# Kernel optimization log

Hardware: AMD Instinct MI355X
Metric: run time of the kernel (lower is better)

## Reference

```python
import jax, jax.numpy as jnp
import numpy as np

N = 50000       # nodes
E = 800000      # edges
D_IN = 128      # input_dim
HID = 256       # hidden_dim
HEADS = 4
FH = HID // 4   # per-head out dim = 64
OUT = 8         # output_dim
NEG_SLOPE = 0.2 # GATConv leaky_relu slope


def setup_inputs() -> dict:
    key = jax.random.key(0)
    ks = jax.random.split(key, 16)
    def glorot(k, shape):
        fan_in, fan_out = shape[0], shape[-1]
        s = jnp.sqrt(6.0 / (fan_in + fan_out))
        return jax.random.uniform(k, shape, jnp.float32, -s, s)
    inp = {
        "x": jax.random.normal(ks[0], (N, D_IN), jnp.float32),
        "edge_index": jax.random.randint(ks[1], (2, E), 0, N, jnp.int64),
        # GCN layers
        "W1": glorot(ks[2], (D_IN, HID)), "b1": jnp.zeros((HID,), jnp.float32),
        "W2": glorot(ks[3], (HID, HID)), "b2": jnp.zeros((HID,), jnp.float32),
        "W3": glorot(ks[4], (HID, HID // 2)), "b3": jnp.zeros((HID // 2,), jnp.float32),
        # GAT layer: in = HID//2 = 128, out per head = FH, 4 heads concat -> HID
        "Wg": glorot(ks[5], (HID // 2, HEADS * FH)),
        "a_src": glorot(ks[6], (HEADS, FH)),
        "a_dst": glorot(ks[7], (HEADS, FH)),
        "bg": jnp.zeros((HEADS * FH,), jnp.float32),
        # classifier MLP: HID -> HID//2 -> HID//4 -> OUT
        "Wc1": glorot(ks[8], (HID, HID // 2)), "bc1": jnp.zeros((HID // 2,), jnp.float32),
        "Wc2": glorot(ks[9], (HID // 2, HID // 4)), "bc2": jnp.zeros((HID // 4,), jnp.float32),
        "Wc3": glorot(ks[10], (HID // 4, OUT)), "bc3": jnp.zeros((OUT,), jnp.float32),
    }
    return inp


def _with_self_loops(edge_index, n):
    loop = jnp.arange(n, dtype=edge_index.dtype)
    src = jnp.concatenate([edge_index[0], loop])
    dst = jnp.concatenate([edge_index[1], loop])
    return src, dst


def gcn_conv(x, W, b, src, dst, n):
    # PyG GCNConv: h = X W; out = D^{-1/2}(A+I)D^{-1/2} h + b (self loops in src/dst)
    h = x @ W
    deg = jax.ops.segment_sum(jnp.ones_like(dst, jnp.float32), dst, num_segments=n)
    dinv = jnp.where(deg > 0, jax.lax.rsqrt(deg), 0.0)
    norm = dinv[src] * dinv[dst]                      # [E+N]
    out = jax.ops.segment_sum(h[src] * norm[:, None], dst, num_segments=n)
    return out + b


def gat_conv(x, Wg, a_src, a_dst, bg, src, dst, n):
    # PyG GATConv (eval mode, no attn dropout), self loops included in src/dst
    h = (x @ Wg).reshape(n, HEADS, FH)                # [N,H,F]
    al_s = jnp.einsum('nhf,hf->nh', h, a_src)         # [N,H]
    al_d = jnp.einsum('nhf,hf->nh', h, a_dst)
    e = jax.nn.leaky_relu(al_s[src] + al_d[dst], NEG_SLOPE)  # [E+N,H]
    m = jax.ops.segment_max(e, dst, num_segments=n)   # per-dst stable softmax
    ex = jnp.exp(e - m[dst])
    den = jax.ops.segment_sum(ex, dst, num_segments=n)
    alpha = ex / den[dst]                             # [E+N,H]
    out = jax.ops.segment_sum(h[src] * alpha[:, :, None], dst, num_segments=n)
    return out.reshape(n, HEADS * FH) + bg


def reference(x, edge_index, W1, b1, W2, b2, W3, b3, Wg, a_src, a_dst, bg,
              Wc1, bc1, Wc2, bc2, Wc3, bc3):
    n = x.shape[0]
    src, dst = _with_self_loops(edge_index, n)
    h1 = jax.nn.relu(gcn_conv(x, W1, b1, src, dst, n))
    h2 = jax.nn.relu(gcn_conv(h1, W2, b2, src, dst, n)) + h1
    h3 = jax.nn.relu(gcn_conv(h2, W3, b3, src, dst, n))
    h_att = jax.nn.relu(gat_conv(h3, Wg, a_src, a_dst, bg, src, dst, n))
    h_pooled = jnp.mean(h_att, axis=0, keepdims=True)           # [1, HID]
    z = jax.nn.relu(h_pooled @ Wc1 + bc1)
    z = jax.nn.relu(z @ Wc2 + bc2)
    return z @ Wc3 + bc3                                        # [1, OUT]
```

## Files before the change

kernel.cpp:

```cpp
#include <hip/hip_runtime.h>
#include <hip/hip_bf16.h>

#define NNODES 50000
#define NEDGES 800000
#define EN 850000
#define SCAN_B 196

typedef __attribute__((ext_vector_type(8))) short bf16x8;
typedef __attribute__((ext_vector_type(4))) float f32x4;

__device__ __forceinline__ float bf2f(unsigned short u) {
    return __uint_as_float(((unsigned)u) << 16);
}
__device__ __forceinline__ float bflo(unsigned u) { return __uint_as_float(u << 16); }
__device__ __forceinline__ float bfhi(unsigned u) { return __uint_as_float(u & 0xffff0000u); }
__device__ __forceinline__ unsigned short f2bf(float x) {
    unsigned u = __float_as_uint(x);
    u += 0x7fffu + ((u >> 16) & 1u);
    return (unsigned short)(u >> 16);
}
__device__ __forceinline__ unsigned pack2bf(float a, float b) {
    return (unsigned)f2bf(a) | ((unsigned)f2bf(b) << 16);
}
__device__ __forceinline__ void acc8(float* acc, uint4 v, float wg) {
    acc[0] += bflo(v.x) * wg; acc[1] += bfhi(v.x) * wg;
    acc[2] += bflo(v.y) * wg; acc[3] += bfhi(v.y) * wg;
    acc[4] += bflo(v.z) * wg; acc[5] += bfhi(v.z) * wg;
    acc[6] += bflo(v.w) * wg; acc[7] += bfhi(v.w) * wg;
}

__device__ __forceinline__ void split_bf(float x, unsigned short& h, unsigned short& l) {
    unsigned u = __float_as_uint(x);
    h = (unsigned short)(u >> 16);
    float r = x - __uint_as_float(u & 0xffff0000u);
    l = (unsigned short)(__float_as_uint(r) >> 16);
}
__device__ __forceinline__ void do_split(const float* W, unsigned short* Wh, unsigned short* Wl,
                                         int i, int K, int N) {
    int n = i / K, k = i - n * K;
    unsigned short h, l;
    split_bf(W[(size_t)k * N + n], h, l);
    Wh[i] = h; Wl[i] = l;
}

__global__ __launch_bounds__(256) void prep_kernel(const int* __restrict__ ei, float* __restrict__ deg,
                                                   const float* __restrict__ x, unsigned short* __restrict__ xbf,
                                                   const float* __restrict__ W1, const float* __restrict__ W2,
                                                   const float* __restrict__ W3, const float* __restrict__ Wg,
                                                   unsigned short* __restrict__ W1th, unsigned short* __restrict__ W1tl,
                                                   unsigned short* __restrict__ W2th, unsigned short* __restrict__ W2tl,
                                                   unsigned short* __restrict__ W3th, unsigned short* __restrict__ W3tl,
                                                   unsigned short* __restrict__ Wgth, unsigned short* __restrict__ Wgtl) {
    int idx = blockIdx.x * 256 + threadIdx.x;
    atomicAdd(&deg[ei[NEDGES + idx]], 1.0f);
    {
        float4 a = *(const float4*)&x[(size_t)idx * 8];
        float4 b = *(const float4*)&x[(size_t)idx * 8 + 4];
        uint4 o;
        o.x = pack2bf(a.x, a.y); o.y = pack2bf(a.z, a.w);
        o.z = pack2bf(b.x, b.y); o.w = pack2bf(b.z, b.w);
        *(uint4*)&xbf[(size_t)idx * 8] = o;
    }
    if (idx < 32768)        do_split(W1, W1th, W1tl, idx, 128, 256);
    else if (idx < 98304)   do_split(W2, W2th, W2tl, idx - 32768, 256, 256);
    else if (idx < 131072)  do_split(W3, W3th, W3tl, idx - 98304, 256, 128);
    else if (idx < 163840)  do_split(Wg, Wgth, Wgtl, idx - 131072, 128, 256);
}

__global__ __launch_bounds__(256) void scan_part1(const float* __restrict__ deg, int* __restrict__ row,
                                                  int* __restrict__ bsum, float* __restrict__ dinv) {
    __shared__ int sdata[256];
    int t = threadIdx.x;
    int idx = blockIdx.x * 256 + t;
    float dg = idx < NNODES ? deg[idx] : 0.f;
    if (idx < NNODES) dinv[idx] = rsqrtf(dg + 1.0f);
    int v = idx < NNODES ? (int)dg + 1 : 0;
    sdata[t] = v;
    __syncthreads();
    for (int off = 1; off < 256; off <<= 1) {
        int tmp = t >= off ? sdata[t - off] : 0;
        __syncthreads();
        sdata[t] += tmp;
        __syncthreads();
    }
    if (idx < NNODES) row[idx] = sdata[t] - v;
    if (t == 255) bsum[blockIdx.x] = sdata[255];
}

__global__ __launch_bounds__(256) void scan_part2(int* __restrict__ bsum, int* __restrict__ bofs,
                                                  int* __restrict__ row) {
    __shared__ int sdata[256];
    int t = threadIdx.x;
    int v = t < SCAN_B ? bsum[t] : 0;
    sdata[t] = v;
    __syncthreads();
    for (int off = 1; off < 256; off <<= 1) {
        int tmp = t >= off ? sdata[t - off] : 0;
        __syncthreads();
        sdata[t] += tmp;
        __syncthreads();
    }
    if (t < SCAN_B) bofs[t] = sdata[t] - v;
    if (t == 0) row[NNODES] = EN;
}

__global__ __launch_bounds__(256) void scan_part3(int* __restrict__ row, const int* __restrict__ bofs) {
    int idx = blockIdx.x * 256 + threadIdx.x;
    if (idx < NNODES) row[idx] += bofs[blockIdx.x];
}

__global__ __launch_bounds__(256) void scatter_kernel(const int* __restrict__ ei, const int* __restrict__ row,
                                                      int* __restrict__ cursor, const float* __restrict__ dinv,
                                                      uint2* __restrict__ csr) {
    int e = blockIdx.x * blockDim.x + threadIdx.x;
    if (e >= EN) return;
    int s, d;
    if (e < NEDGES) { s = ei[e]; d = ei[NEDGES + e]; } else { s = e - NEDGES; d = s; }
    int pos = row[d] + atomicAdd(&cursor[d], 1);
    csr[pos] = make_uint2((unsigned)s, __float_as_uint(dinv[s] * dinv[d]));
}

template<int MODE>
__global__ __launch_bounds__(256) void gemm_bf(const unsigned short* __restrict__ A,
                                               const unsigned short* __restrict__ Wth,
                                               const unsigned short* __restrict__ Wtl,
                                               const float* __restrict__ bias,
                                               const float* __restrict__ asr, const float* __restrict__ ads,
                                               float* __restrict__ als, float* __restrict__ ald,
                                               unsigned short* __restrict__ C, int M, int K, int Nc) {
    __shared__ unsigned short As[128][40];
    __shared__ unsigned short Bh[128][40], Bl[128][40];
    int t = threadIdx.x;
    int row0 = blockIdx.x * 128, col0 = blockIdx.y * 128;
    int lane = t & 63, w = t >> 6;
    int mb = (w >> 1) * 64, nb = (w & 1) * 64;
    int lr = lane & 15, kg = (lane >> 4) * 8;

    f32x4 acc[4][4];
#pragma unroll
    for (int i = 0; i < 4; ++i)
#pragma unroll
        for (int j = 0; j < 4; ++j) acc[i][j] = (f32x4){0.f, 0.f, 0.f, 0.f};

    for (int k0 = 0; k0 < K; k0 += 32) {
#pragma unroll
        for (int it = 0; it < 2; ++it) {
            int q = it * 256 + t;
            int row = q >> 2, seg = (q & 3) * 8;
            int grow = row0 + row;
            uint4 v = make_uint4(0, 0, 0, 0);
            if (grow < M) v = *(const uint4*)&A[(size_t)grow * K + k0 + seg];
            *(uint4*)&As[row][seg] = v;
        }
#pragma unroll
        for (int it = 0; it < 2; ++it) {
            int o = it * 256 + t;
            int n = o >> 2, ko = (o & 3) * 8;
            size_t g = (size_t)(col0 + n) * K + k0 + ko;
            *(uint4*)&Bh[n][ko] = *(const uint4*)&Wth[g];
            *(uint4*)&Bl[n][ko] = *(const uint4*)&Wtl[g];
        }
        __syncthreads();

        bf16x8 a[4], bh[4], bl[4];
#pragma unroll
        for (int mf = 0; mf < 4; ++mf) a[mf] = *(const bf16x8*)&As[mb + mf * 16 + lr][kg];
#pragma unroll
        for (int nf = 0; nf < 4; ++nf) {
            bh[nf] = *(const bf16x8*)&Bh[nb + nf * 16 + lr][kg];
            bl[nf] = *(const bf16x8*)&Bl[nb + nf * 16 + lr][kg];
        }
#pragma unroll
        for (int mf = 0; mf < 4; ++mf)
#pragma unroll
            for (int nf = 0; nf < 4; ++nf) {
                acc[mf][nf] = __builtin_amdgcn_mfma_f32_16x16x32_bf16(a[mf], bh[nf], acc[mf][nf], 0, 0, 0);
                acc[mf][nf] = __builtin_amdgcn_mfma_f32_16x16x32_bf16(a[mf], bl[nf], acc[mf][nf], 0, 0, 0);
            }
        __syncthreads();
    }

    float s1[16], s2[16];
    if (MODE == 2) {
#pragma unroll
        for (int q = 0; q < 16; ++q) { s1[q] = 0.f; s2[q] = 0.f; }
    }

#pragma unroll
    for (int nf = 0; nf < 4; ++nf) {
        int col = col0 + nb + nf * 16 + lr;
        float bv = (MODE == 1) ? bias[col] : 0.f;
        float av = 0.f, dv = 0.f;
        if (MODE == 2) { av = asr[col]; dv = ads[col]; }
#pragma unroll
        for (int mf = 0; mf < 4; ++mf) {
#pragma unroll
            for (int r = 0; r < 4; ++r) {
                int row = row0 + mb + mf * 16 + (lane >> 4) * 4 + r;
                if (row < M) {
                    float v = acc[mf][nf][r];
                    if (MODE == 1) v = fmaxf(v + bv, 0.f);
                    C[(size_t)row * Nc + col] = f2bf(v);
                    if (MODE == 2) {
                        s1[mf * 4 + r] += v * av;
                        s2[mf * 4 + r] += v * dv;
                    }
                }
            }
        }
    }
    if (MODE == 2) {
        int head = (col0 + nb) >> 6;
#pragma unroll
        for (int q = 0; q < 16; ++q) {
#pragma unroll
            for (int off = 1; off < 16; off <<= 1) {
                s1[q] += __shfl_xor(s1[q], off);
                s2[q] += __shfl_xor(s2[q], off);
            }
        }
        if (lr == 0) {
#pragma unroll
            for (int mf = 0; mf < 4; ++mf) {
#pragma unroll
                for (int r = 0; r < 4; ++r) {
                    int row = row0 + mb + mf * 16 + (lane >> 4) * 4 + r;
                    if (row < M) {
                        als[row * 4 + head] = s1[mf * 4 + r];
                        ald[row * 4 + head] = s2[mf * 4 + r];
                    }
                }
            }
        }
    }
}

template<int NC, int MODE>
__global__ __launch_bounds__(256) void gcn_agg_bf(const unsigned short* __restrict__ h, const int* __restrict__ row,
                                                  const uint2* __restrict__ csr,
                                                  const float* __restrict__ b, const unsigned short* __restrict__ res,
                                                  unsigned short* __restrict__ out) {
    int wid = (int)((blockIdx.x * blockDim.x + threadIdx.x) >> 6);
    if (wid >= NNODES) return;
    int lane = threadIdx.x & 63;
    constexpr int LPE = NC / 8;
    constexpr int EPI = 64 / LPE;
    int sub = lane / LPE, li = lane % LPE;
    int col = li * 8;
    float acc[8];
#pragma unroll
    for (int i = 0; i < 8; ++i) acc[i] = 0.f;
    int j0 = row[wid], j1 = row[wid + 1];
    int j = j0 + sub;
    for (; j + 3 * EPI < j1; j += 4 * EPI) {
        uint2 c0 = csr[j], c1 = csr[j + EPI], c2 = csr[j + 2 * EPI], c3 = csr[j + 3 * EPI];
        uint4 v0 = *(const uint4*)&h[(size_t)c0.x * NC + col];
        uint4 v1 = *(const uint4*)&h[(size_t)c1.x * NC + col];
        uint4 v2 = *(const uint4*)&h[(size_t)c2.x * NC + col];
        uint4 v3 = *(const uint4*)&h[(size_t)c3.x * NC + col];
        acc8(acc, v0, __uint_as_float(c0.y));
        acc8(acc, v1, __uint_as_float(c1.y));
        acc8(acc, v2, __uint_as_float(c2.y));
        acc8(acc, v3, __uint_as_float(c3.y));
    }
    for (; j < j1; j += EPI) {
        uint2 c0 = csr[j];
        uint4 v0 = *(const uint4*)&h[(size_t)c0.x * NC + col];
        acc8(acc, v0, __uint_as_float(c0.y));
    }
#pragma unroll
    for (int i = 0; i < 8; ++i) {
        acc[i] += __shfl_xor(acc[i], 32);
        if constexpr (EPI == 4) acc[i] += __shfl_xor(acc[i], 16);
    }
    if (lane < LPE) {
        if constexpr (MODE >= 1) {
#pragma unroll
            for (int i = 0; i < 8; ++i) acc[i] = fmaxf(acc[i] + b[col + i], 0.f);
        }
        if constexpr (MODE == 2) {
            uint4 rv = *(const uint4*)&res[(size_t)wid * NC + col];
            acc8(acc, rv, 1.0f);
        }
        uint4 o;
        o.x = pack2bf(acc[0], acc[1]); o.y = pack2bf(acc[2], acc[3]);
        o.z = pack2bf(acc[4], acc[5]); o.w = pack2bf(acc[6], acc[7]);
        *(uint4*)&out[(size_t)wid * NC + col] = o;
    }
}

__device__ __forceinline__ float lrelu(float x) { return x < 0.f ? 0.2f * x : x; }

__global__ __launch_bounds__(256) void gat_csr(const unsigned short* __restrict__ hg, const int* __restrict__ row,
                                               const uint2* __restrict__ csr, const float* __restrict__ als,
                                               const float* __restrict__ ald, const float* __restrict__ bg,
                                               unsigned short* __restrict__ out) {
    __shared__ float alds[4][64][4];
    int wid = (int)((blockIdx.x * blockDim.x + threadIdx.x) >> 6);
    if (wid >= NNODES) return;
    int wv = threadIdx.x >> 6;
    int lane = threadIdx.x & 63;
    int j0 = row[wid], j1 = row[wid + 1];
    int deg = j1 - j0;
    float4 ad = *(const float4*)&ald[wid * 4];
    int sub = lane >> 5, li = lane & 31;
    int h = li >> 3;
    int col = li * 8;
    float acc[8];
#pragma unroll
    for (int i = 0; i < 8; ++i) acc[i] = 0.f;

    if (deg <= 64) {
        int sreg = 0;
        float e0 = -1e30f, e1 = -1e30f, e2 = -1e30f, e3 = -1e30f;
        if (lane < deg) {
            sreg = (int)csr[j0 + lane].x;
            float4 as4 = *(const float4*)&als[sreg * 4];
            e0 = lrelu(as4.x + ad.x); e1 = lrelu(as4.y + ad.y);
            e2 = lrelu(as4.z + ad.z); e3 = lrelu(as4.w + ad.w);
        }
        float m0 = e0, m1 = e1, m2 = e2, m3 = e3;
#pragma unroll
        for (int off = 32; off >= 1; off >>= 1) {
            m0 = fmaxf(m0, __shfl_xor(m0, off));
            m1 = fmaxf(m1, __shfl_xor(m1, off));
            m2 = fmaxf(m2, __shfl_xor(m2, off));
            m3 = fmaxf(m3, __shfl_xor(m3, off));
        }
        float x0 = __expf(e0 - m0), x1 = __expf(e1 - m1);
        float x2 = __expf(e2 - m2), x3 = __expf(e3 - m3);
        float d0 = x0, d1 = x1, d2 = x2, d3 = x3;
#pragma unroll
        for (int off = 32; off >= 1; off >>= 1) {
            d0 += __shfl_xor(d0, off);
            d1 += __shfl_xor(d1, off);
            d2 += __shfl_xor(d2, off);
            d3 += __shfl_xor(d3, off);
        }
        float i0 = 1.f / d0, i1 = 1.f / d1, i2 = 1.f / d2, i3 = 1.f / d3;
        *(float4*)&alds[wv][lane][0] = make_float4(x0 * i0, x1 * i1, x2 * i2, x3 * i3);
        int k = sub;
        for (; k + 6 < deg; k += 8) {
            int s0 = __shfl(sreg, k),     s1 = __shfl(sreg, k + 2);
            int s2 = __shfl(sreg, k + 4), s3 = __shfl(sreg, k + 6);
            float a0 = alds[wv][k][h],     a1 = alds[wv][k + 2][h];
            float a2 = alds[wv][k + 4][h], a3 = alds[wv][k + 6][h];
            uint4 v0 = *(const uint4*)&hg[(size_t)s0 * 256 + col];
            uint4 v1 = *(const uint4*)&hg[(size_t)s1 * 256 + col];
            uint4 v2 = *(const uint4*)&hg[(size_t)s2 * 256 + col];
            uint4 v3 = *(const uint4*)&hg[(size_t)s3 * 256 + col];
            acc8(acc, v0, a0); acc8(acc, v1, a1);
            acc8(acc, v2, a2); acc8(acc, v3, a3);
        }
        for (; k < deg; k += 2) {
            int s0 = __shfl(sreg, k);
            float a0 = alds[wv][k][h];
            uint4 v0 = *(const uint4*)&hg[(size_t)s0 * 256 + col];
            acc8(acc, v0, a0);
        }
    } else {
        float m0 = -1e30f, m1 = -1e30f, m2 = -1e30f, m3 = -1e30f;
        float d0 = 0.f, d1 = 0.f, d2 = 0.f, d3 = 0.f;
        for (int j = j0 + lane; j < j1; j += 64) {
            int s = (int)csr[j].x;
            float4 as4 = *(const float4*)&als[s * 4];
            m0 = fmaxf(m0, lrelu(as4.x + ad.x));
            m1 = fmaxf(m1, lrelu(as4.y + ad.y));
            m2 = fmaxf(m2, lrelu(as4.z + ad.z));
            m3 = fmaxf(m3, lrelu(as4.w + ad.w));
        }
#pragma unroll
        for (int off = 32; off >= 1; off >>= 1) {
            m0 = fmaxf(m0, __shfl_xor(m0, off));
            m1 = fmaxf(m1, __shfl_xor(m1, off));
            m2 = fmaxf(m2, __shfl_xor(m2, off));
            m3 = fmaxf(m3, __shfl_xor(m3, off));
        }
        for (int j = j0 + lane; j < j1; j += 64) {
            int s = (int)csr[j].x;
            float4 as4 = *(const float4*)&als[s * 4];
            d0 += __expf(lrelu(as4.x + ad.x) - m0);
            d1 += __expf(lrelu(as4.y + ad.y) - m1);
            d2 += __expf(lrelu(as4.z + ad.z) - m2);
            d3 += __expf(lrelu(as4.w + ad.w) - m3);
        }
#pragma unroll
        for (int off = 32; off >= 1; off >>= 1) {
            d0 += __shfl_xor(d0, off);
            d1 += __shfl_xor(d1, off);
            d2 += __shfl_xor(d2, off);
            d3 += __shfl_xor(d3, off);
        }
        float mh   = h == 0 ? m0 : h == 1 ? m1 : h == 2 ? m2 : m3;
        float invh = 1.f / (h == 0 ? d0 : h == 1 ? d1 : h == 2 ? d2 : d3);
        float adh  = h == 0 ? ad.x : h == 1 ? ad.y : h == 2 ? ad.z : ad.w;
        for (int j = j0 + sub; j < j1; j += 2) {
            uint2 c0 = csr[j];
            float a0 = __expf(lrelu(als[c0.x * 4 + h] + adh) - mh) * invh;
            uint4 v0 = *(const uint4*)&hg[(size_t)c0.x * 256 + col];
            acc8(acc, v0, a0);
        }
    }

#pragma unroll
    for (int i = 0; i < 8; ++i) acc[i] += __shfl_xor(acc[i], 32);
    if (lane < 32) {
        uint4 o;
        o.x = pack2bf(fmaxf(acc[0] + bg[col], 0.f),     fmaxf(acc[1] + bg[col + 1], 0.f));
        o.y = pack2bf(fmaxf(acc[2] + bg[col + 2], 0.f), fmaxf(acc[3] + bg[col + 3], 0.f));
        o.z = pack2bf(fmaxf(acc[4] + bg[col + 4], 0.f), fmaxf(acc[5] + bg[col + 5], 0.f));
        o.w = pack2bf(fmaxf(acc[6] + bg[col + 6], 0.f), fmaxf(acc[7] + bg[col + 7], 0.f));
        *(uint4*)&out[(size_t)wid * 256 + col] = o;
    }
}

__global__ __launch_bounds__(256) void pool_kernel(const unsigned short* __restrict__ hatt, float* __restrict__ ppart) {
    int col = threadIdx.x;
    int r0 = blockIdx.x * 256;
    int r1 = r0 + 256 < NNODES ? r0 + 256 : NNODES;
    float s = 0.f;
    for (int r = r0; r < r1; ++r) s += bf2f(hatt[(size_t)r * 256 + col]);
    ppart[blockIdx.x * 256 + col] = s;
}

__global__ __launch_bounds__(256) void mlp_kernel(const float* __restrict__ ppart,
                                                  const float* __restrict__ Wc1, const float* __restrict__ bc1,
                                                  const float* __restrict__ Wc2, const float* __restrict__ bc2,
                                                  const float* __restrict__ Wc3, const float* __restrict__ bc3,
                                                  float* __restrict__ out) {
    __shared__ float p[256], z1[128], z2[64];
    int t = threadIdx.x;
    float s0 = 0.f;
    for (int b = 0; b < SCAN_B; ++b) s0 += ppart[b * 256 + t];
    p[t] = s0 * (1.0f / NNODES);
    __syncthreads();
    if (t < 128) {
        float s = bc1[t];
        for (int k = 0; k < 256; ++k) s += p[k] * Wc1[k * 128 + t];
        z1[t] = fmaxf(s, 0.f);
    }
    __syncthreads();
    if (t < 64) {
        float s = bc2[t];
        for (int k = 0; k < 128; ++k) s += z1[k] * Wc2[k * 64 + t];
        z2[t] = fmaxf(s, 0.f);
    }
    __syncthreads();
    if (t < 8) {
        float s = bc3[t];
        for (int k = 0; k < 64; ++k) s += z2[k] * Wc3[k * 8 + t];
        out[t] = s;
    }
}

extern "C" void kernel_launch(void* const* d_in, const int* in_sizes, int n_in,
                              void* d_out, int out_size, void* d_ws, size_t ws_size,
                              hipStream_t stream) {
    const float* x   = (const float*)d_in[0];
    const int*   ei  = (const int*)d_in[1];
    const float* W1  = (const float*)d_in[2];  const float* b1  = (const float*)d_in[3];
    const float* W2  = (const float*)d_in[4];  const float* b2  = (const float*)d_in[5];
    const float* W3  = (const float*)d_in[6];  const float* b3  = (const float*)d_in[7];
    const float* Wg  = (const float*)d_in[8];
    const float* asr = (const float*)d_in[9];  const float* ads = (const float*)d_in[10];
    const float* bg  = (const float*)d_in[11];
    const float* Wc1 = (const float*)d_in[12]; const float* bc1 = (const float*)d_in[13];
    const float* Wc2 = (const float*)d_in[14]; const float* bc2 = (const float*)d_in[15];
    const float* Wc3 = (const float*)d_in[16]; const float* bc3 = (const float*)d_in[17];
    float* out = (float*)d_out;

    char* w = (char*)d_ws;
    float* deg    = (float*)w; w += (size_t)NNODES * 4;
    int*   cursor = (int*)w;   w += (size_t)NNODES * 4;
    float* dinv   = (float*)w; w += (size_t)NNODES * 4;
    int*   rowp   = (int*)w;   w += 200016;
    int*   bsum   = (int*)w;   w += 256 * 4;
    int*   bofs   = (int*)w;   w += 256 * 4;
    uint2* csr    = (uint2*)w; w += (size_t)EN * 8;
    float* als    = (float*)w; w += (size_t)NNODES * 4 * 4;
    float* ald    = (float*)w; w += (size_t)NNODES * 4 * 4;
    float* ppart  = (float*)w; w += (size_t)SCAN_B * 256 * 4;
    unsigned short* W1th = (unsigned short*)w; w += 128 * 256 * 2;
    unsigned short* W1tl = (unsigned short*)w; w += 128 * 256 * 2;
    unsigned short* W2th = (unsigned short*)w; w += 256 * 256 * 2;
    unsigned short* W2tl = (unsigned short*)w; w += 256 * 256 * 2;
    unsigned short* W3th = (unsigned short*)w; w += 256 * 128 * 2;
    unsigned short* W3tl = (unsigned short*)w; w += 256 * 128 * 2;
    unsigned short* Wgth = (unsigned short*)w; w += 128 * 256 * 2;
    unsigned short* Wgtl = (unsigned short*)w; w += 128 * 256 * 2;
    unsigned short* U1 = (unsigned short*)w; w += (size_t)NNODES * 256 * 2;
    unsigned short* U2 = (unsigned short*)w; w += (size_t)NNODES * 256 * 2;
    unsigned short* U3 = (unsigned short*)w; w += (size_t)NNODES * 256 * 2;
    unsigned short* U4 = (unsigned short*)w; w += (size_t)NNODES * 256 * 2;

    hipMemsetAsync(deg, 0, (size_t)NNODES * 8, stream);
    prep_kernel<<<3125, 256, 0, stream>>>(ei, deg, x, U1, W1, W2, W3, Wg,
                                          W1th, W1tl, W2th, W2tl, W3th, W3tl, Wgth, Wgtl);
    scan_part1<<<SCAN_B, 256, 0, stream>>>(deg, rowp, bsum, dinv);
    scan_part2<<<1, 256, 0, stream>>>(bsum, bofs, rowp);
    scan_part3<<<SCAN_B, 256, 0, stream>>>(rowp, bofs);
    scatter_kernel<<<(EN + 255) / 256, 256, 0, stream>>>(ei, rowp, cursor, dinv, csr);

    dim3 gA((NNODES + 127) / 128, 2);
    dim3 gB((NNODES + 127) / 128, 1);
    int aggBlocks = (NNODES * 64 + 255) / 256;

    gcn_agg_bf<128, 0><<<aggBlocks, 256, 0, stream>>>(U1, rowp, csr, nullptr, nullptr, U2);
    gemm_bf<1><<<gA, 256, 0, stream>>>(U2, W1th, W1tl, b1, nullptr, nullptr, nullptr, nullptr, U3, NNODES, 128, 256);

    gemm_bf<0><<<gA, 256, 0, stream>>>(U3, W2th, W2tl, nullptr, nullptr, nullptr, nullptr, nullptr, U1, NNODES, 256, 256);
    gcn_agg_bf<256, 2><<<aggBlocks, 256, 0, stream>>>(U1, rowp, csr, b2, U3, U2);

    gemm_bf<0><<<gB, 256, 0, stream>>>(U2, W3th, W3tl, nullptr, nullptr, nullptr, nullptr, nullptr, U4, NNODES, 256, 128);
    gcn_agg_bf<128, 1><<<aggBlocks, 256, 0, stream>>>(U4, rowp, csr, b3, nullptr, U1);

    gemm_bf<2><<<gA, 256, 0, stream>>>(U1, Wgth, Wgtl, nullptr, asr, ads, als, ald, U2, NNODES, 128, 256);
    gat_csr<<<aggBlocks, 256, 0, stream>>>(U2, rowp, csr, als, ald, bg, U3);

    pool_kernel<<<SCAN_B, 256, 0, stream>>>(U3, ppart);
    mlp_kernel<<<1, 256, 0, stream>>>(ppart, Wc1, bc1, Wc2, bc2, Wc3, bc3, out);
}
```

Measured before the change: 533.2 us.

## Reorder GAT layer to aggregate before projection, fold attention vectors into weights

The GAT layer is reassociated. Attention logits are computed directly from h3 using precomputed Wg·a_src and Wg·a_dst vectors, fused into the third GCN aggregation. Per-head weighted aggregation then runs over the 128-wide h3 rather than the 256-wide projected features, and a per-head GEMM with bias and relu follows. This removes the gather of 256-wide rows in GAT and the logit epilogue in the GEMM. In exchange it writes a 4x128-wide intermediate P and does more FMAs per edge. The scan_part3 launch is also dropped by adding block offsets at use sites.

```diff
diff --git a/kernel.cpp b/kernel.cpp
--- a/kernel.cpp
+++ b/kernel.cpp
@@ -28,6 +28,15 @@
     acc[4] += bflo(v.z) * wg; acc[5] += bfhi(v.z) * wg;
     acc[6] += bflo(v.w) * wg; acc[7] += bfhi(v.w) * wg;
 }
+__device__ __forceinline__ void accP(float (&a4)[4][8], uint4 v, float4 al) {
+    float f[8] = {bflo(v.x), bfhi(v.x), bflo(v.y), bfhi(v.y),
+                  bflo(v.z), bfhi(v.z), bflo(v.w), bfhi(v.w)};
+#pragma unroll
+    for (int i = 0; i < 8; ++i) {
+        a4[0][i] += f[i] * al.x; a4[1][i] += f[i] * al.y;
+        a4[2][i] += f[i] * al.z; a4[3][i] += f[i] * al.w;
+    }
+}
 
 __device__ __forceinline__ void split_bf(float x, unsigned short& h, unsigned short& l) {
     unsigned u = __float_as_uint(x);
@@ -47,10 +56,12 @@
                                                    const float* __restrict__ x, unsigned short* __restrict__ xbf,
                                                    const float* __restrict__ W1, const float* __restrict__ W2,
                                                    const float* __restrict__ W3, const float* __restrict__ Wg,
+                                                   const float* __restrict__ asr, const float* __restrict__ ads,
                                                    unsigned short* __restrict__ W1th, unsigned short* __restrict__ W1tl,
                                                    unsigned short* __restrict__ W2th, unsigned short* __restrict__ W2tl,
                                                    unsigned short* __restrict__ W3th, unsigned short* __restrict__ W3tl,
-                                                   unsigned short* __restrict__ Wgth, unsigned short* __restrict__ Wgtl) {
+                                                   unsigned short* __restrict__ Wgth, unsigned short* __restrict__ Wgtl,
+                                                   float* __restrict__ asp, float* __restrict__ adp) {
     int idx = blockIdx.x * 256 + threadIdx.x;
     atomicAdd(&deg[ei[NEDGES + idx]], 1.0f);
     {
@@ -65,6 +76,18 @@
     else if (idx < 98304)   do_split(W2, W2th, W2tl, idx - 32768, 256, 256);
     else if (idx < 131072)  do_split(W3, W3th, W3tl, idx - 98304, 256, 128);
     else if (idx < 163840)  do_split(Wg, Wgth, Wgtl, idx - 131072, 128, 256);
+    else if (idx < 164864) {
+        int i0 = idx - 163840;
+        int which = i0 >> 9;
+        int h = (i0 >> 7) & 3;
+        int k = i0 & 127;
+        const float* av = (which ? ads : asr) + h * 64;
+        const float* wg = Wg + (size_t)k * 256 + h * 64;
+        float s = 0.f;
+#pragma unroll
+        for (int c = 0; c < 64; ++c) s += wg[c] * av[c];
+        (which ? adp : asp)[h * 128 + k] = s;
+    }
 }
 
 __global__ __launch_bounds__(256) void scan_part1(const float* __restrict__ deg, int* __restrict__ row,
@@ -101,22 +124,18 @@
         __syncthreads();
     }
     if (t < SCAN_B) bofs[t] = sdata[t] - v;
-    if (t == 0) row[NNODES] = EN;
-}
-
-__global__ __launch_bounds__(256) void scan_part3(int* __restrict__ row, const int* __restrict__ bofs) {
-    int idx = blockIdx.x * 256 + threadIdx.x;
-    if (idx < NNODES) row[idx] += bofs[blockIdx.x];
+    if (t == SCAN_B - 1) row[NNODES] = EN - (sdata[t] - v);
 }
 
 __global__ __launch_bounds__(256) void scatter_kernel(const int* __restrict__ ei, const int* __restrict__ row,
+                                                      const int* __restrict__ bofs,
                                                       int* __restrict__ cursor, const float* __restrict__ dinv,
                                                       uint2* __restrict__ csr) {
     int e = blockIdx.x * blockDim.x + threadIdx.x;
     if (e >= EN) return;
     int s, d;
     if (e < NEDGES) { s = ei[e]; d = ei[NEDGES + e]; } else { s = e - NEDGES; d = s; }
-    int pos = row[d] + atomicAdd(&cursor[d], 1);
+    int pos = row[d] + bofs[d >> 8] + atomicAdd(&cursor[d], 1);
     csr[pos] = make_uint2((unsigned)s, __float_as_uint(dinv[s] * dinv[d]));
 }
 
@@ -125,8 +144,6 @@
                                                const unsigned short* __restrict__ Wth,
                                                const unsigned short* __restrict__ Wtl,
                                                const float* __restrict__ bias,
-                                               const float* __restrict__ asr, const float* __restrict__ ads,
-                                               float* __restrict__ als, float* __restrict__ ald,
                                                unsigned short* __restrict__ C, int M, int K, int Nc) {
     __shared__ unsigned short As[128][40];
     __shared__ unsigned short Bh[128][40], Bl[128][40];
@@ -180,18 +197,10 @@
         __syncthreads();
     }
 
-    float s1[16], s2[16];
-    if (MODE == 2) {
-#pragma unroll
-        for (int q = 0; q < 16; ++q) { s1[q] = 0.f; s2[q] = 0.f; }
-    }
-
 #pragma unroll
     for (int nf = 0; nf < 4; ++nf) {
         int col = col0 + nb + nf * 16 + lr;
         float bv = (MODE == 1) ? bias[col] : 0.f;
-        float av = 0.f, dv = 0.f;
-        if (MODE == 2) { av = asr[col]; dv = ads[col]; }
 #pragma unroll
         for (int mf = 0; mf < 4; ++mf) {
 #pragma unroll
@@ -201,35 +210,82 @@
                     float v = acc[mf][nf][r];
                     if (MODE == 1) v = fmaxf(v + bv, 0.f);
                     C[(size_t)row * Nc + col] = f2bf(v);
-                    if (MODE == 2) {
-                        s1[mf * 4 + r] += v * av;
-                        s2[mf * 4 + r] += v * dv;
-                    }
                 }
             }
         }
     }
-    if (MODE == 2) {
-        int head = (col0 + nb) >> 6;
-#pragma unroll
-        for (int q = 0; q < 16; ++q) {
-#pragma unroll
-            for (int off = 1; off < 16; off <<= 1) {
-                s1[q] += __shfl_xor(s1[q], off);
-                s2[q] += __shfl_xor(s2[q], off);
+}
+
+__global__ __launch_bounds__(256) void gemm_head(const unsigned short* __restrict__ P,
+                                                 const unsigned short* __restrict__ Wgth,
+                                                 const unsigned short* __restrict__ Wgtl,
+                                                 const float* __restrict__ bg,
+                                                 unsigned short* __restrict__ C) {
+    __shared__ unsigned short As[128][40];
+    __shared__ unsigned short Bh[64][40], Bl[64][40];
+    int t = threadIdx.x;
+    int head = blockIdx.y;
+    int row0 = blockIdx.x * 128;
+    const unsigned short* A  = P + (size_t)head * NNODES * 128;
+    const unsigned short* Wh = Wgth + head * 64 * 128;
+    const unsigned short* Wl = Wgtl + head * 64 * 128;
+    int lane = t & 63, w = t >> 6;
+    int mb = w * 32;
+    int lr = lane & 15, kg = (lane >> 4) * 8;
+
+    f32x4 acc[2][4];
+#pragma unroll
+    for (int i = 0; i < 2; ++i)
+#pragma unroll
+        for (int j = 0; j < 4; ++j) acc[i][j] = (f32x4){0.f, 0.f, 0.f, 0.f};
+
+    for (int k0 = 0; k0 < 128; k0 += 32) {
+#pragma unroll
+        for (int it = 0; it < 2; ++it) {
+            int q = it * 256 + t;
+            int row = q >> 2, seg = (q & 3) * 8;
+            int grow = row0 + row;
+            uint4 v = make_uint4(0, 0, 0, 0);
+            if (grow < NNODES) v = *(const uint4*)&A[(size_t)grow * 128 + k0 + seg];
+            *(uint4*)&As[row][seg] = v;
+        }
+        {
+            int n = t >> 2, ko = (t & 3) * 8;
+            size_t g = (size_t)n * 128 + k0 + ko;
+            *(uint4*)&Bh[n][ko] = *(const uint4*)&Wh[g];
+            *(uint4*)&Bl[n][ko] = *(const uint4*)&Wl[g];
+        }
+        __syncthreads();
+
+        bf16x8 a[2], bh[4], bl[4];
+#pragma unroll
+        for (int mf = 0; mf < 2; ++mf) a[mf] = *(const bf16x8*)&As[mb + mf * 16 + lr][kg];
+#pragma unroll
+        for (int nf = 0; nf < 4; ++nf) {
+            bh[nf] = *(const bf16x8*)&Bh[nf * 16 + lr][kg];
+            bl[nf] = *(const bf16x8*)&Bl[nf * 16 + lr][kg];
+        }
+#pragma unroll
+        for (int mf = 0; mf < 2; ++mf)
+#pragma unroll
+            for (int nf = 0; nf < 4; ++nf) {
+                acc[mf][nf] = __builtin_amdgcn_mfma_f32_16x16x32_bf16(a[mf], bh[nf], acc[mf][nf], 0, 0, 0);
+                acc[mf][nf] = __builtin_amdgcn_mfma_f32_16x16x32_bf16(a[mf], bl[nf], acc[mf][nf], 0, 0, 0);
             }
-        }
-        if (lr == 0) {
-#pragma unroll
-            for (int mf = 0; mf < 4; ++mf) {
-#pragma unroll
-                for (int r = 0; r < 4; ++r) {
-                    int row = row0 + mb + mf * 16 + (lane >> 4) * 4 + r;
-                    if (row < M) {
-                        als[row * 4 + head] = s1[mf * 4 + r];
-                        ald[row * 4 + head] = s2[mf * 4 + r];
-                    }
-                }
+        __syncthreads();
+    }
+
+#pragma unroll
+    for (int nf = 0; nf < 4; ++nf) {
+        int gcol = head * 64 + nf * 16 + lr;
+        float bv = bg[gcol];
+#pragma unroll
+        for (int mf = 0; mf < 2; ++mf) {
+#pragma unroll
+            for (int r = 0; r < 4; ++r) {
+                int row = row0 + mb + mf * 16 + (lane >> 4) * 4 + r;
+                if (row < NNODES)
+                    C[(size_t)row * 256 + gcol] = f2bf(fmaxf(acc[mf][nf][r] + bv, 0.f));
             }
         }
     }
@@ -237,8 +293,10 @@
 
 template<int NC, int MODE>
 __global__ __launch_bounds__(256) void gcn_agg_bf(const unsigned short* __restrict__ h, const int* __restrict__ row,
-                                                  const uint2* __restrict__ csr,
+                                                  const int* __restrict__ bofs, const uint2* __restrict__ csr,
                                                   const float* __restrict__ b, const unsigned short* __restrict__ res,
+                                                  const float* __restrict__ asp, const float* __restrict__ adp,
+                                                  float* __restrict__ als, float* __restrict__ ald,
                                                   unsigned short* __restrict__ out) {
     int wid = (int)((blockIdx.x * blockDim.x + threadIdx.x) >> 6);
     if (wid >= NNODES) return;
@@ -250,7 +308,8 @@
     float acc[8];
 #pragma unroll
     for (int i = 0; i < 8; ++i) acc[i] = 0.f;
-    int j0 = row[wid], j1 = row[wid + 1];
+    int j0 = row[wid] + bofs[wid >> 8];
+    int j1 = row[wid + 1] + bofs[(wid + 1) >> 8];
     int j = j0 + sub;
     for (; j + 3 * EPI < j1; j += 4 * EPI) {
         uint2 c0 = csr[j], c1 = csr[j + EPI], c2 = csr[j + 2 * EPI], c3 = csr[j + 3 * EPI];
@@ -286,29 +345,56 @@
         o.x = pack2bf(acc[0], acc[1]); o.y = pack2bf(acc[2], acc[3]);
         o.z = pack2bf(acc[4], acc[5]); o.w = pack2bf(acc[6], acc[7]);
         *(uint4*)&out[(size_t)wid * NC + col] = o;
+        if constexpr (MODE == 3) {
+            float s1[4], s2[4];
+#pragma unroll
+            for (int hh = 0; hh < 4; ++hh) {
+                float t1 = 0.f, t2 = 0.f;
+#pragma unroll
+                for (int i = 0; i < 8; ++i) {
+                    t1 += acc[i] * asp[hh * 128 + col + i];
+                    t2 += acc[i] * adp[hh * 128 + col + i];
+                }
+                s1[hh] = t1; s2[hh] = t2;
+            }
+#pragma unroll
+            for (int off = 1; off <= 8; off <<= 1) {
+#pragma unroll
+                for (int hh = 0; hh < 4; ++hh) {
+                    s1[hh] += __shfl_xor(s1[hh], off);
+                    s2[hh] += __shfl_xor(s2[hh], off);
+                }
+            }
+            if (lane == 0) {
+                *(float4*)&als[wid * 4] = make_float4(s1[0], s1[1], s1[2], s1[3]);
+                *(float4*)&ald[wid * 4] = make_float4(s2[0], s2[1], s2[2], s2[3]);
+            }
+        }
     }
 }
 
 __device__ __forceinline__ float lrelu(float x) { return x < 0.f ? 0.2f * x : x; }
 
-__global__ __launch_bounds__(256) void gat_csr(const unsigned short* __restrict__ hg, const int* __restrict__ row,
-                                               const uint2* __restrict__ csr, const float* __restrict__ als,
-                                               const float* __restrict__ ald, const float* __restrict__ bg,
-                                               unsigned short* __restrict__ out) {
+__global__ __launch_bounds__(256) void gat_agg(const unsigned short* __restrict__ h3, const int* __restrict__ row,
+                                               const int* __restrict__ bofs, const uint2* __restrict__ csr,
+                                               const float* __restrict__ als, const float* __restrict__ ald,
+                                               unsigned short* __restrict__ P) {
     __shared__ float alds[4][64][4];
     int wid = (int)((blockIdx.x * blockDim.x + threadIdx.x) >> 6);
     if (wid >= NNODES) return;
     int wv = threadIdx.x >> 6;
     int lane = threadIdx.x & 63;
-    int j0 = row[wid], j1 = row[wid + 1];
+    int j0 = row[wid] + bofs[wid >> 8];
+    int j1 = row[wid + 1] + bofs[(wid + 1) >> 8];
     int deg = j1 - j0;
     float4 ad = *(const float4*)&ald[wid * 4];
-    int sub = lane >> 5, li = lane & 31;
-    int h = li >> 3;
+    int sub = lane >> 4, li = lane & 15;
     int col = li * 8;
-    float acc[8];
-#pragma unroll
-    for (int i = 0; i < 8; ++i) acc[i] = 0.f;
+    float a4[4][8];
+#pragma unroll
+    for (int hh = 0; hh < 4; ++hh)
+#pragma unroll
+        for (int i = 0; i < 8; ++i) a4[hh][i] = 0.f;
 
     if (deg <= 64) {
         int sreg = 0;
@@ -337,26 +423,22 @@
             d2 += __shfl_xor(d2, off);
             d3 += __shfl_xor(d3, off);
         }
-        float i0 = 1.f / d0, i1 = 1.f / d1, i2 = 1.f / d2, i3 = 1.f / d3;
-        *(float4*)&alds[wv][lane][0] = make_float4(x0 * i0, x1 * i1, x2 * i2, x3 * i3);
+        *(float4*)&alds[wv][lane][0] = make_float4(x0 / d0, x1 / d1, x2 / d2, x3 / d3);
         int k = sub;
-        for (; k + 6 < deg; k += 8) {
-            int s0 = __shfl(sreg, k),     s1 = __shfl(sreg, k + 2);
-            int s2 = __shfl(sreg, k + 4), s3 = __shfl(sreg, k + 6);
-            float a0 = alds[wv][k][h],     a1 = alds[wv][k + 2][h];
-            float a2 = alds[wv][k + 4][h], a3 = alds[wv][k + 6][h];
-            uint4 v0 = *(const uint4*)&hg[(size_t)s0 * 256 + col];
-            uint4 v1 = *(const uint4*)&hg[(size_t)s1 * 256 + col];
-            uint4 v2 = *(const uint4*)&hg[(size_t)s2 * 256 + col];
-            uint4 v3 = *(const uint4*)&hg[(size_t)s3 * 256 + col];
-            acc8(acc, v0, a0); acc8(acc, v1, a1);
-            acc8(acc, v2, a2); acc8(acc, v3, a3);
-        }
-        for (; k < deg; k += 2) {
+        for (; k + 4 < deg; k += 8) {
+            int s0 = __shfl(sreg, k), s1 = __shfl(sreg, k + 4);
+            float4 al0 = *(const float4*)&alds[wv][k][0];
+            float4 al1 = *(const float4*)&alds[wv][k + 4][0];
+            uint4 v0 = *(const uint4*)&h3[(size_t)s0 * 128 + col];
+            uint4 v1 = *(const uint4*)&h3[(size_t)s1 * 128 + col];
+            accP(a4, v0, al0);
+            accP(a4, v1, al1);
+        }
+        if (k < deg) {
             int s0 = __shfl(sreg, k);
-            float a0 = alds[wv][k][h];
-            uint4 v0 = *(const uint4*)&hg[(size_t)s0 * 256 + col];
-            acc8(acc, v0, a0);
+            float4 al0 = *(const float4*)&alds[wv][k][0];
+            uint4 v0 = *(const uint4*)&h3[(size_t)s0 * 128 + col];
+            accP(a4, v0, al0);
         }
     } else {
         float m0 = -1e30f, m1 = -1e30f, m2 = -1e30f, m3 = -1e30f;
@@ -391,26 +473,35 @@
             d2 += __shfl_xor(d2, off);
             d3 += __shfl_xor(d3, off);
         }
-        float mh   = h == 0 ? m0 : h == 1 ? m1 : h == 2 ? m2 : m3;
-        float invh = 1.f / (h == 0 ? d0 : h == 1 ? d1 : h == 2 ? d2 : d3);
-        float adh  = h == 0 ? ad.x : h == 1 ? ad.y : h == 2 ? ad.z : ad.w;
-        for (int j = j0 + sub; j < j1; j += 2) {
-            uint2 c0 = csr[j];
-            float a0 = __expf(lrelu(als[c0.x * 4 + h] + adh) - mh) * invh;
-            uint4 v0 = *(const uint4*)&hg[(size_t)c0.x * 256 + col];
-            acc8(acc, v0, a0);
-        }
-    }
-
-#pragma unroll
-    for (int i = 0; i < 8; ++i) acc[i] += __shfl_xor(acc[i], 32);
-    if (lane < 32) {
-        uint4 o;
-        o.x = pack2bf(fmaxf(acc[0] + bg[col], 0.f),     fmaxf(acc[1] + bg[col + 1], 0.f));
-        o.y = pack2bf(fmaxf(acc[2] + bg[col + 2], 0.f), fmaxf(acc[3] + bg[col + 3], 0.f));
-        o.z = pack2bf(fmaxf(acc[4] + bg[col + 4], 0.f), fmaxf(acc[5] + bg[col + 5], 0.f));
-        o.w = pack2bf(fmaxf(acc[6] + bg[col + 6], 0.f), fmaxf(acc[7] + bg[col + 7], 0.f));
-        *(uint4*)&out[(size_t)wid * 256 + col] = o;
+        float i0 = 1.f / d0, i1 = 1.f / d1, i2 = 1.f / d2, i3 = 1.f / d3;
+        for (int j = j0 + sub; j < j1; j += 4) {
+            uint2 c = csr[j];
+            float4 as4 = *(const float4*)&als[c.x * 4];
+            float4 al;
+            al.x = __expf(lrelu(as4.x + ad.x) - m0) * i0;
+            al.y = __expf(lrelu(as4.y + ad.y) - m1) * i1;
+            al.z = __expf(lrelu(as4.z + ad.z) - m2) * i2;
+            al.w = __expf(lrelu(as4.w + ad.w) - m3) * i3;
+            uint4 v = *(const uint4*)&h3[(size_t)c.x * 128 + col];
+            accP(a4, v, al);
+        }
+    }
+
+#pragma unroll
+    for (int hh = 0; hh < 4; ++hh)
+#pragma unroll
+        for (int i = 0; i < 8; ++i) {
+            a4[hh][i] += __shfl_xor(a4[hh][i], 16);
+            a4[hh][i] += __shfl_xor(a4[hh][i], 32);
+        }
+    if (lane < 16) {
+#pragma unroll
+        for (int hh = 0; hh < 4; ++hh) {
+            uint4 o;
+            o.x = pack2bf(a4[hh][0], a4[hh][1]); o.y = pack2bf(a4[hh][2], a4[hh][3]);
+            o.z = pack2bf(a4[hh][4], a4[hh][5]); o.w = pack2bf(a4[hh][6], a4[hh][7]);
+            *(uint4*)&P[((size_t)hh * NNODES + wid) * 128 + col] = o;
+        }
     }
 }
 
@@ -480,6 +571,8 @@
     float* als    = (float*)w; w += (size_t)NNODES * 4 * 4;
     float* ald    = (float*)w; w += (size_t)NNODES * 4 * 4;
     float* ppart  = (float*)w; w += (size_t)SCAN_B * 256 * 4;
+    float* asp    = (float*)w; w += 4 * 128 * 4;
+    float* adp    = (float*)w; w += 4 * 128 * 4;
     unsigned short* W1th = (unsigned short*)w; w += 128 * 256 * 2;
     unsigned short* W1tl = (unsigned short*)w; w += 128 * 256 * 2;
     unsigned short* W2th = (unsigned short*)w; w += 256 * 256 * 2;
@@ -492,31 +585,35 @@
     unsigned short* U2 = (unsigned short*)w; w += (size_t)NNODES * 256 * 2;
     unsigned short* U3 = (unsigned short*)w; w += (size_t)NNODES * 256 * 2;
     unsigned short* U4 = (unsigned short*)w; w += (size_t)NNODES * 256 * 2;
+    unsigned short* P  = (unsigned short*)w; w += (size_t)4 * NNODES * 128 * 2;
 
     hipMemsetAsync(deg, 0, (size_t)NNODES * 8, stream);
-    prep_kernel<<<3125, 256, 0, stream>>>(ei, deg, x, U1, W1, W2, W3, Wg,
-                                          W1th, W1tl, W2th, W2tl, W3th, W3tl, Wgth, Wgtl);
+    prep_kernel<<<3125, 256, 0, stream>>>(ei, deg, x, U1, W1, W2, W3, Wg, asr, ads,
+                                          W1th, W1tl, W2th, W2tl, W3th, W3tl, Wgth, Wgtl, asp, adp);
     scan_part1<<<SCAN_B, 256, 0, stream>>>(deg, rowp, bsum, dinv);
     scan_part2<<<1, 256, 0, stream>>>(bsum, bofs, rowp);
-    scan_part3<<<SCAN_B, 256, 0, stream>>>(rowp, bofs);
-    scatter_kernel<<<(EN + 255) / 256, 256, 0, stream>>>(ei, rowp, cursor, dinv, csr);
+    scatter_kernel<<<(EN + 255) / 256, 256, 0, stream>>>(ei, rowp, bofs, cursor, dinv, csr);
 
     dim3 gA((NNODES + 127) / 128, 2);
     dim3 gB((NNODES + 127) / 128, 1);
+    dim3 gH((NNODES + 127) / 128, 4);
     int aggBlocks = (NNODES * 64 + 255) / 256;
 
-    gcn_agg_bf<128, 0><<<aggBlocks, 256, 0, stream>>>(U1, rowp, csr, nullptr, nullptr, U2);
-    gemm_bf<1><<<gA, 256, 0, stream>>>(U2, W1th, W1tl, b1, nullptr, nullptr, nullptr, nullptr, U3, NNODES, 128, 256);
-
-    gemm_bf<0><<<gA, 256, 0, stream>>>(U3, W2th, W2tl, nullptr, nullptr, nullptr, nullptr, nullptr, U1, NNODES, 256, 256);
-    gcn_agg_bf<256, 2><<<aggBlocks, 256, 0, stream>>>(U1, rowp, csr, b2, U3, U2);
-
-    gemm_bf<0><<<gB, 256, 0, stream>>>(U2, W3th, W3tl, nullptr, nullptr, nullptr, nullptr, nullptr, U4, NNODES, 256, 128);
-    gcn_agg_bf<128, 1><<<aggBlocks, 256, 0, stream>>>(U4, rowp, csr, b3, nullptr, U1);
-
-    gemm_bf<2><<<gA, 256, 0, stream>>>(U1, Wgth, Wgtl, nullptr, asr, ads, als, ald, U2, NNODES, 128, 256);
-    gat_csr<<<aggBlocks, 256, 0, stream>>>(U2, rowp, csr, als, ald, bg, U3);
-
-    pool_kernel<<<SCAN_B, 256, 0, stream>>>(U3, ppart);
+    gcn_agg_bf<128, 0><<<aggBlocks, 256, 0, stream>>>(U1, rowp, bofs, csr, nullptr, nullptr,
+                                                      nullptr, nullptr, nullptr, nullptr, U2);
+    gemm_bf<1><<<gA, 256, 0, stream>>>(U2, W1th, W1tl, b1, U3, NNODES, 128, 256);
+
+    gemm_bf<0><<<gA, 256, 0, stream>>>(U3, W2th, W2tl, nullptr, U1, NNODES, 256, 256);
+    gcn_agg_bf<256, 2><<<aggBlocks, 256, 0, stream>>>(U1, rowp, bofs, csr, b2, U3,
+                                                      nullptr, nullptr, nullptr, nullptr, U2);
+
+    gemm_bf<0><<<gB, 256, 0, stream>>>(U2, W3th, W3tl, nullptr, U4, NNODES, 256, 128);
+    gcn_agg_bf<128, 3><<<aggBlocks, 256, 0, stream>>>(U4, rowp, bofs, csr, b3, nullptr,
+                                                      asp, adp, als, ald, U1);
+
+    gat_agg<<<aggBlocks, 256, 0, stream>>>(U1, rowp, bofs, csr, als, ald, P);
+    gemm_head<<<gH, 256, 0, stream>>>(P, Wgth, Wgtl, bg, U2);
+
+    pool_kernel<<<SCAN_B, 256, 0, stream>>>(U2, ppart);
     mlp_kernel<<<1, 256, 0, stream>>>(ppart, Wc1, bc1, Wc2, bc2, Wc3, bc3, out);
 }
```

Measured after the change: 548.8 us. 2.9% more time.
